# Performance work log

Measured on AMD Instinct MI355X. Metric: run time of the kernel, lower is better.

The kernel has to match this reference:

```python
import jax, jax.numpy as jnp
import numpy as np

H = W = 1024
CHUNK = 32  # rows per chunk in the column EDT pass (keeps intermediate at 32*H*W floats)


def setup_inputs() -> dict:
    key = jax.random.key(0)
    k1, k2 = jax.random.split(key)
    preds = jax.random.randint(k1, (H, W), 0, 2).astype(jnp.float32)
    targets = jax.random.randint(k2, (H, W), 0, 2).astype(jnp.float32)
    return {"preds": preds, "targets": targets}


def _edges(seg):
    # morphological erosion via 3x3 box conv, threshold at 9 == kernel.numel()
    s = seg[None, None]  # (1,1,H,W)
    kern = jnp.ones((1, 1, 3, 3), seg.dtype)
    conv = jax.lax.conv_general_dilated(s, kern, (1, 1), ((1, 1), (1, 1)))
    eroded = (conv[0, 0] == 9.0).astype(seg.dtype)
    return seg - eroded


def _edt(edges):
    # exact Euclidean distance transform: distance to nearest zero of (1 - edges),
    # i.e. nearest pixel where edges == 1.  Separable exact algorithm:
    #   1) per-row 1D distance to nearest feature (via cummax/cummin scans)
    #   2) per-column lower envelope min_k g2[k,j] + (i-k)^2 (chunked brute force)
    feat = (1.0 - edges) == 0.0
    Hh, Ww = edges.shape
    BIG = jnp.float32(1e6)
    col = jnp.arange(Ww, dtype=jnp.float32)
    left = col - jax.lax.cummax(jnp.where(feat, col, -BIG), axis=1)
    right = jax.lax.cummin(jnp.where(feat, col, BIG), axis=1, reverse=True) - col
    g = jnp.minimum(jnp.minimum(left, right), BIG)  # row-wise 1D distance
    g2 = g * g  # (H,W) squared row distances
    rows = jnp.arange(Hh, dtype=jnp.float32)

    def chunk(ic):  # ic: (CHUNK,) target row indices
        # (CHUNK, H, W): g2[k,j] + (i-k)^2, min over source row k
        d = g2[None, :, :] + (ic[:, None, None] - rows[None, :, None]) ** 2
        return jnp.min(d, axis=1)  # (CHUNK, W)

    D2 = jax.lax.map(chunk, rows.reshape(-1, CHUNK)).reshape(Hh, Ww)
    return jnp.sqrt(D2)


def reference(preds, targets):
    pred_edges = _edges(preds)
    target_edges = _edges(targets)
    # scipy EDT ran on detached CPU copies -> no gradient through the DTs
    pred_dt = jax.lax.stop_gradient(_edt(pred_edges))
    target_dt = jax.lax.stop_gradient(_edt(target_edges))
    pred_err = target_edges * pred_dt
    target_err = pred_edges * target_dt
    loss = (jnp.mean(pred_err) + jnp.mean(target_err)) / 2.0
    return jax.nn.sigmoid(loss)
```

## Files before the change

kernel.cpp:

```cpp
#include <hip/hip_runtime.h>
#include <math.h>


#define HW 1024
#define WIN 8
#define RPB 64
#define KROWS (RPB + 2 * WIN)
#define HS_STRIDE 17
#define NC (RPB + 18)
#define NW (RPB + 2)
#define NROWS (NC + NW)
#define NSLOT (NROWS * 8)

__device__ inline int edge_at(const float* __restrict__ seg, int k, int j)
{
    if ((unsigned)k >= (unsigned)HW || (unsigned)j >= (unsigned)HW) return 0;
    if (seg[k * HW + j] == 0.f) return 0;
    bool all9 = true;
    #pragma unroll
    for (int dy = -1; dy <= 1; ++dy)
        #pragma unroll
        for (int dx = -1; dx <= 1; ++dx) {
            const int kk = k + dy, jj = j + dx;
            const float v = ((unsigned)kk < (unsigned)HW && (unsigned)jj < (unsigned)HW)
                            ? seg[kk * HW + jj] : 0.f;
            all9 = all9 && (v != 0.f);
        }
    return all9 ? 0 : 1;
}

__global__ __launch_bounds__(256)
void k_main(const float* __restrict__ pred, const float* __restrict__ targ,
            float* __restrict__ partial)
{
    const int t   = threadIdx.x;
    const int bid = blockIdx.x;
    const int xcd = bid & 7;
    const int sub = bid >> 3;
    const int jt  = sub & 63;
    const int r2  = sub >> 6;
    const int mc  = r2 & 1;
    const int it  = xcd * 2 + (r2 >> 1);
    const int j0 = jt * 16;
    const int i0 = it * RPB;
    const float* __restrict__ segc = mc ? targ : pred;
    const float* __restrict__ segw = mc ? pred : targ;

    __shared__ unsigned s_m[NROWS];
    __shared__ float hs[KROWS * HS_STRIDE];
    __shared__ unsigned short esb[RPB];
    __shared__ float wsum[4];

    const int W0 = j0 - 8;

    #pragma unroll
    for (int itr = 0; itr < 5; ++itr) {
        const int idx = t + itr * 256;
        unsigned partm = 0;
        int row = -1;
        if (idx < NSLOT) {
            row = idx >> 3;
            const int c4 = idx & 7;
            const int isW = row >= NC;
            const int gr  = isW ? (i0 - 1 + (row - NC)) : (i0 - 9 + row);
            const int c   = W0 + c4 * 4;
            float4 v = make_float4(0.f, 0.f, 0.f, 0.f);
            if ((unsigned)gr < (unsigned)HW && (unsigned)c <= 1020u) {
                const float* __restrict__ base = isW ? segw : segc;
                v = *(const float4*)&base[gr * HW + c];
            }
            const unsigned by = (unsigned)(v.x != 0.f) | ((unsigned)(v.y != 0.f) << 1)
                              | ((unsigned)(v.z != 0.f) << 2) | ((unsigned)(v.w != 0.f) << 3);
            partm = by << (4 * c4);
        }
        partm |= __shfl_xor(partm, 1);
        partm |= __shfl_xor(partm, 2);
        partm |= __shfl_xor(partm, 4);
        if (idx < NSLOT && (t & 7) == 0) s_m[row] = partm;
    }
    __syncthreads();

    if (t < RPB) {
        const unsigned sA = s_m[NC + t], sB = s_m[NC + t + 1], sC = s_m[NC + t + 2];
        const unsigned va = sA & sB & sC;
        const unsigned er = va & (va << 1) & (va >> 1);
        const unsigned edge = sB & ~er;
        esb[t] = (unsigned short)((edge >> 8) & 0xFFFFu);
    }
    if (t < KROWS) {
        const int kr = i0 - WIN + t;
        float* __restrict__ hrow = &hs[t * HS_STRIDE];
        if ((unsigned)kr < (unsigned)HW) {
            const unsigned sA = s_m[t], sB = s_m[t + 1], sC = s_m[t + 2];
            const unsigned va = sA & sB & sC;
            const unsigned er = va & (va << 1) & (va >> 1);
            const unsigned edge = (sB & ~er) & 0x7FFFFFFEu;
            const float krk = (float)(kr * kr);
            #pragma unroll
            for (int jc = 0; jc < 16; ++jc) {
                const int p = 8 + jc;
                const unsigned mle = edge & ((1u << (p + 1)) - 1u);
                const unsigned mge = edge >> p;
                int g = 1 << 20;
                if (mle) g = p - (31 - __clz(mle));
                if (mge) g = min(g, __ffs(mge) - 1);
                hrow[jc] = (g < (1 << 20)) ? fmaf((float)g, (float)g, krk) : 1e30f;
            }
        } else {
            #pragma unroll
            for (int jc = 0; jc < 16; ++jc) hrow[jc] = 1e30f;
        }
    }
    __syncthreads();

    const int jj = t & 15;
    const int iw = t >> 4;
    float lsum = 0.f;
    {
        const int ib = i0 + iw * 4;
        const int kkS = iw * 4;
        float b0 = 3e38f, b1 = 3e38f, b2 = 3e38f, b3 = 3e38f;
        float kf = (float)(ib - WIN);
        const float m0 = -2.f * (float)(ib);
        const float m1 = -2.f * (float)(ib + 1);
        const float m2 = -2.f * (float)(ib + 2);
        const float m3 = -2.f * (float)(ib + 3);
        #pragma unroll
        for (int kk = kkS; kk < kkS + 2 * WIN + 4; ++kk) {
            const float hvv = hs[kk * HS_STRIDE + jj];
            b0 = fminf(b0, fmaf(m0, kf, hvv));
            b1 = fminf(b1, fmaf(m1, kf, hvv));
            b2 = fminf(b2, fmaf(m2, kf, hvv));
            b3 = fminf(b3, fmaf(m3, kf, hvv));
            kf += 1.f;
        }
        const int sLo = max(0, ib - WIN);
        const int sHi = min(HW - 1, ib + WIN + 3);
        float bs[4] = {b0, b1, b2, b3};
        #pragma unroll
        for (int w = 0; w < 4; ++w) {
            const int i = ib + w;
            float D2 = (float)(i * i) + bs[w];
            const int dl = i - sLo + 1, dr = sHi + 1 - i;
            const bool need = (D2 > 64.f) ||
                              ((sLo > 0) && (D2 > (float)(dl * dl))) ||
                              ((sHi < HW - 1) && (D2 > (float)(dr * dr)));
            if (need) {
                const int jg = j0 + jj;
                float bb = 1e6f - (float)jg;
                bb = bb * bb;
                for (int k = 0; k < HW; ++k) {
                    const float rowt = (float)((i - k) * (i - k));
                    if (rowt >= bb) continue;
                    for (int d = 0; d < HW; ++d) {
                        const float dd = rowt + (float)(d * d);
                        if (dd >= bb) break;
                        if (edge_at(segc, k, jg - d) || edge_at(segc, k, jg + d)) {
                            bb = dd; break;
                        }
                    }
                }
                D2 = bb;
            }
            const unsigned wbit = (esb[i - i0] >> jj) & 1u;
            lsum += wbit ? sqrtf(D2) : 0.f;
        }
    }

    #pragma unroll
    for (int off = 32; off > 0; off >>= 1) lsum += __shfl_down(lsum, off);
    if ((t & 63) == 0) wsum[t >> 6] = lsum;
    __syncthreads();
    if (t == 0)
        partial[bid] = wsum[0] + wsum[1] + wsum[2] + wsum[3];
}

__global__ __launch_bounds__(256)
void k_fin(const float* __restrict__ partial, float* __restrict__ out)
{
    const int t = threadIdx.x;
    float s = 0.f;
    #pragma unroll
    for (int q = 0; q < 8; ++q) s += partial[t + q * 256];
    #pragma unroll
    for (int off = 32; off > 0; off >>= 1) s += __shfl_down(s, off);
    __shared__ float w[4];
    if ((t & 63) == 0) w[t >> 6] = s;
    __syncthreads();
    if (t == 0) {
        const float tot = w[0] + w[1] + w[2] + w[3];
        const float loss = tot * (1.f / (2.f * 1024.f * 1024.f));
        out[0] = 1.f / (1.f + expf(-loss));
    }
}

extern "C" void kernel_launch(void* const* d_in, const int* in_sizes, int n_in,
                              void* d_out, int out_size, void* d_ws, size_t ws_size,
                              hipStream_t stream)
{
    const float* preds   = (const float*)d_in[0];
    const float* targets = (const float*)d_in[1];
    float* out = (float*)d_out;

    float* partial = (float*)d_ws;

    k_main<<<dim3(2048), 256, 0, stream>>>(preds, targets, partial);
    k_fin<<<1, 256, 0, stream>>>(partial, out);
}
```

Before: 68.96 us.

## Fuse final reduction into main kernel via last-block atomic counter, batch loads

Removes the separate finalization kernel: each block publishes its partial sum atomically and increments a global counter, and the last block to finish sums all partials and writes the sigmoid loss. A memset of the counter is added before the launch. The mask-building loop is also split so all five float4 global loads are issued before any bit packing, to raise memory-level parallelism. This trades one kernel launch for a memset plus atomic traffic and a serialized tail in the last block.

```diff
diff --git a/kernel.cpp b/kernel.cpp
--- a/kernel.cpp
+++ b/kernel.cpp
@@ -11,6 +11,7 @@
 #define NW (RPB + 2)
 #define NROWS (NC + NW)
 #define NSLOT (NROWS * 8)
+#define NBLK 2048
 
 __device__ inline int edge_at(const float* __restrict__ seg, int k, int j)
 {
@@ -31,7 +32,8 @@
 
 __global__ __launch_bounds__(256)
 void k_main(const float* __restrict__ pred, const float* __restrict__ targ,
-            float* __restrict__ partial)
+            float* __restrict__ partial, unsigned* __restrict__ counter,
+            float* __restrict__ out)
 {
     const int t   = threadIdx.x;
     const int bid = blockIdx.x;
@@ -50,33 +52,46 @@
     __shared__ float hs[KROWS * HS_STRIDE];
     __shared__ unsigned short esb[RPB];
     __shared__ float wsum[4];
+    __shared__ int s_last;
 
     const int W0 = j0 - 8;
 
+    float4 v[5];
+    int rowA[5];
     #pragma unroll
     for (int itr = 0; itr < 5; ++itr) {
         const int idx = t + itr * 256;
-        unsigned partm = 0;
-        int row = -1;
+        v[itr] = make_float4(0.f, 0.f, 0.f, 0.f);
+        rowA[itr] = 0;
         if (idx < NSLOT) {
-            row = idx >> 3;
+            const int row = idx >> 3;
+            rowA[itr] = row;
             const int c4 = idx & 7;
             const int isW = row >= NC;
             const int gr  = isW ? (i0 - 1 + (row - NC)) : (i0 - 9 + row);
             const int c   = W0 + c4 * 4;
-            float4 v = make_float4(0.f, 0.f, 0.f, 0.f);
             if ((unsigned)gr < (unsigned)HW && (unsigned)c <= 1020u) {
                 const float* __restrict__ base = isW ? segw : segc;
-                v = *(const float4*)&base[gr * HW + c];
+                v[itr] = *(const float4*)&base[gr * HW + c];
             }
-            const unsigned by = (unsigned)(v.x != 0.f) | ((unsigned)(v.y != 0.f) << 1)
-                              | ((unsigned)(v.z != 0.f) << 2) | ((unsigned)(v.w != 0.f) << 3);
+        }
+    }
+    #pragma unroll
+    for (int itr = 0; itr < 5; ++itr) {
+        const int idx = t + itr * 256;
+        unsigned partm = 0;
+        if (idx < NSLOT) {
+            const int c4 = idx & 7;
+            const unsigned by = (unsigned)(v[itr].x != 0.f)
+                              | ((unsigned)(v[itr].y != 0.f) << 1)
+                              | ((unsigned)(v[itr].z != 0.f) << 2)
+                              | ((unsigned)(v[itr].w != 0.f) << 3);
             partm = by << (4 * c4);
         }
         partm |= __shfl_xor(partm, 1);
         partm |= __shfl_xor(partm, 2);
         partm |= __shfl_xor(partm, 4);
-        if (idx < NSLOT && (t & 7) == 0) s_m[row] = partm;
+        if (idx < NSLOT && (t & 7) == 0) s_m[rowA[itr]] = partm;
     }
     __syncthreads();
 
@@ -171,26 +186,31 @@
     for (int off = 32; off > 0; off >>= 1) lsum += __shfl_down(lsum, off);
     if ((t & 63) == 0) wsum[t >> 6] = lsum;
     __syncthreads();
-    if (t == 0)
-        partial[bid] = wsum[0] + wsum[1] + wsum[2] + wsum[3];
-}
-
-__global__ __launch_bounds__(256)
-void k_fin(const float* __restrict__ partial, float* __restrict__ out)
-{
-    const int t = threadIdx.x;
-    float s = 0.f;
-    #pragma unroll
-    for (int q = 0; q < 8; ++q) s += partial[t + q * 256];
-    #pragma unroll
-    for (int off = 32; off > 0; off >>= 1) s += __shfl_down(s, off);
-    __shared__ float w[4];
-    if ((t & 63) == 0) w[t >> 6] = s;
-    __syncthreads();
+
     if (t == 0) {
-        const float tot = w[0] + w[1] + w[2] + w[3];
-        const float loss = tot * (1.f / (2.f * 1024.f * 1024.f));
-        out[0] = 1.f / (1.f + expf(-loss));
+        const float ps = wsum[0] + wsum[1] + wsum[2] + wsum[3];
+        __hip_atomic_store(&partial[bid], ps, __ATOMIC_RELAXED,
+                           __HIP_MEMORY_SCOPE_AGENT);
+        const unsigned old = __hip_atomic_fetch_add(counter, 1u, __ATOMIC_ACQ_REL,
+                                                    __HIP_MEMORY_SCOPE_AGENT);
+        s_last = (old == (unsigned)(NBLK - 1));
+    }
+    __syncthreads();
+    if (s_last) {
+        float s = 0.f;
+        #pragma unroll
+        for (int q = 0; q < 8; ++q)
+            s += __hip_atomic_load(&partial[t + q * 256], __ATOMIC_RELAXED,
+                                   __HIP_MEMORY_SCOPE_AGENT);
+        #pragma unroll
+        for (int off = 32; off > 0; off >>= 1) s += __shfl_down(s, off);
+        if ((t & 63) == 0) wsum[t >> 6] = s;
+        __syncthreads();
+        if (t == 0) {
+            const float tot = wsum[0] + wsum[1] + wsum[2] + wsum[3];
+            const float loss = tot * (1.f / (2.f * 1024.f * 1024.f));
+            out[0] = 1.f / (1.f + expf(-loss));
+        }
     }
 }
 
@@ -202,8 +222,9 @@
     const float* targets = (const float*)d_in[1];
     float* out = (float*)d_out;
 
-    float* partial = (float*)d_ws;
-
-    k_main<<<dim3(2048), 256, 0, stream>>>(preds, targets, partial);
-    k_fin<<<1, 256, 0, stream>>>(partial, out);
+    float* partial    = (float*)d_ws;
+    unsigned* counter = (unsigned*)((char*)d_ws + 8192);
+
+    hipMemsetAsync(counter, 0, sizeof(unsigned), stream);
+    k_main<<<dim3(NBLK), 256, 0, stream>>>(preds, targets, partial, counter, out);
 }
```

Result: slower. 104.4 us (+51.4%).
